# Kernel tuning notes

Hardware: AMD Instinct MI355X
Metric: run time of the kernel (lower is better)

## Reference

```python
import jax, jax.numpy as jnp
import numpy as np
from jax import lax

H = 512   # hidden_size
R = 4     # read heads
W = 32    # memory word size
N = 64    # memory cells
B = 64    # batch
T = 256   # seq len
IFACE = R * W + 3 * W + 5 * R + 3      # 247
HID_C = H + IFACE                       # 759 controller LSTM hidden
IN_C = H + R * W                        # 640 controller LSTM input
EPS = 1e-6


def setup_inputs() -> dict:
    key = jax.random.key(0)
    ks = jax.random.split(key, 7)
    s = 0.05
    return {
        "x": jax.random.normal(ks[0], (B, T, H), jnp.float32),
        "Wih_e": jax.random.normal(ks[1], (4 * H, H), jnp.float32) * s,
        "Whh_e": jax.random.normal(ks[2], (4 * H, H), jnp.float32) * s,
        "b_e": jnp.zeros((4 * H,), jnp.float32),
        "Wih_c": jax.random.normal(ks[3], (4 * HID_C, IN_C), jnp.float32) * s,
        "Whh_c": jax.random.normal(ks[4], (4 * HID_C, HID_C), jnp.float32) * s,
        "b_c": jnp.zeros((4 * HID_C,), jnp.float32),
    }


def lstm_cell(xt, h, c, Wih, Whh, b):
    g = xt @ Wih.T + h @ Whh.T + b
    i, f, gg, o = jnp.split(g, 4, axis=-1)  # PyTorch gate order i,f,g,o
    c = jax.nn.sigmoid(f) * c + jax.nn.sigmoid(i) * jnp.tanh(gg)
    h = jax.nn.sigmoid(o) * jnp.tanh(c)
    return h, c


def content_weights(M, keys, strengths):
    # M: [B,N,W], keys: [B,K,W], strengths: [B,K] -> softmaxed similarity [B,K,N]
    Mn = M * lax.rsqrt(jnp.sum(M * M, -1, keepdims=True) + EPS)
    kn = keys * lax.rsqrt(jnp.sum(keys * keys, -1, keepdims=True) + EPS)
    sim = jnp.einsum('bkw,bnw->bkn', kn, Mn)
    return jax.nn.softmax(sim * strengths[..., None], axis=-1)


def reference(x, Wih_e, Whh_e, b_e, Wih_c, Whh_c, b_c):
    # ---- encoder LSTM over time ----
    def enc_step(carry, xt):
        h, c = carry
        h, c = lstm_cell(xt, h, c, Wih_e, Whh_e, b_e)
        return (h, c), h

    z = jnp.zeros((B, H), x.dtype)
    _, enc = lax.scan(enc_step, (z, z), x.transpose(1, 0, 2))  # [T,B,H]

    # ---- controller LSTM + DNC memory per timestep ----
    eye = jnp.eye(N, dtype=x.dtype)

    def dnc_step(carry, e_t):
        h, c, M, u, p, L, wr, ww, rv = carry
        x_t = jnp.concatenate([e_t, rv], axis=-1)          # [B, H + R*W]
        h, c = lstm_cell(x_t, h, c, Wih_c, Whh_c, b_c)
        out = h[:, :H]
        xi = h[:, H:]                                       # [B, IFACE]
        o = 0
        read_keys = jnp.tanh(xi[:, :R * W].reshape(B, R, W)); o = R * W
        read_str = jax.nn.softplus(xi[:, o:o + R]); o += R
        write_key = jnp.tanh(xi[:, o:o + W]).reshape(B, 1, W); o += W
        write_str = jax.nn.softplus(xi[:, o:o + 1]); o += 1
        erase = jax.nn.sigmoid(xi[:, o:o + W]); o += W
        write_vec = jnp.tanh(xi[:, o:o + W]); o += W
        free_g = jax.nn.sigmoid(xi[:, o:o + R]); o += R
        alloc_g = jax.nn.sigmoid(xi[:, o:o + 1]); o += 1
        write_g = jax.nn.sigmoid(xi[:, o:o + 1]); o += 1
        read_modes = jax.nn.softmax(xi[:, o:o + 3 * R].reshape(B, R, 3), -1)
        # usage + retention
        psi = jnp.prod(1.0 - free_g[..., None] * wr, axis=1)   # [B,N]
        u = (u + ww - u * ww) * psi
        # allocation weighting via sorted usage
        idx = jnp.argsort(u, axis=-1)
        su = jnp.take_along_axis(u, idx, -1)
        cp = jnp.concatenate([jnp.ones((B, 1), u.dtype), jnp.cumprod(su, -1)[:, :-1]], -1)
        a = jnp.take_along_axis((1.0 - su) * cp, jnp.argsort(idx, -1), -1)
        # write weighting
        cw = content_weights(M, write_key, write_str)[:, 0]    # [B,N]
        ww = write_g * (alloc_g * a + (1.0 - alloc_g) * cw)
        # memory write
        M = M * (1.0 - ww[..., None] * erase[:, None, :]) + ww[..., None] * write_vec[:, None, :]
        # temporal link + precedence
        L = (1.0 - ww[:, :, None] - ww[:, None, :]) * L + ww[:, :, None] * p[:, None, :]
        L = L * (1.0 - eye)
        p = (1.0 - jnp.sum(ww, -1, keepdims=True)) * p + ww
        # read weighting: backward, content, forward modes
        cr = content_weights(M, read_keys, read_str)           # [B,R,N]
        fw = jnp.einsum('bnm,brm->brn', L, wr)
        bw = jnp.einsum('bmn,brm->brn', L, wr)
        wr = read_modes[..., 0:1] * bw + read_modes[..., 1:2] * cr + read_modes[..., 2:3] * fw
        rv = jnp.einsum('brn,bnw->brw', wr, M).reshape(B, R * W)
        return (h, c, M, u, p, L, wr, ww, rv), out

    init = (
        jnp.zeros((B, HID_C), x.dtype), jnp.zeros((B, HID_C), x.dtype),
        jnp.zeros((B, N, W), x.dtype), jnp.zeros((B, N), x.dtype),
        jnp.zeros((B, N), x.dtype), jnp.zeros((B, N, N), x.dtype),
        jnp.zeros((B, R, N), x.dtype), jnp.zeros((B, N), x.dtype),
        jnp.zeros((B, R * W), x.dtype),
    )
    _, outs = lax.scan(dnc_step, init, enc)   # [T,B,H]
    return outs.transpose(1, 0, 2)            # dnc_encoded [B,T,H]
```

## Files before the change

kernel.cpp:

```cpp
#include <hip/hip_runtime.h>
#include <math.h>


#define EPSF 1e-6f

__device__ __forceinline__ float sigmoidf_(float x) { return 1.f / (1.f + expf(-x)); }
__device__ __forceinline__ float softplusf_(float x) {
    return (x > 0.f) ? x + log1pf(expf(-x)) : log1pf(expf(x));
}
__device__ __forceinline__ void stg_coh(float* p, float v) {
    __hip_atomic_store(p, v, __ATOMIC_RELAXED, __HIP_MEMORY_SCOPE_AGENT);
}
__device__ __forceinline__ void st_flag(int* p, int v) {
    __hip_atomic_store(p, v, __ATOMIC_RELAXED, __HIP_MEMORY_SCOPE_AGENT);
}
__device__ __forceinline__ int ld_flag(const int* p) {
    return __hip_atomic_load(p, __ATOMIC_RELAXED, __HIP_MEMORY_SCOPE_AGENT);
}
__device__ __forceinline__ void poll256(const int* f, int lane, int tgt) {
    const int* p = f + lane * 32;
    for (;;) {
        int a = ld_flag(p);
        int b = ld_flag(p + 64 * 32);
        int c = ld_flag(p + 128 * 32);
        int d = ld_flag(p + 192 * 32);
        if (__all(min(min(a, b), min(c, d)) >= tgt)) break;
        __builtin_amdgcn_s_sleep(2);
    }
}
__device__ __forceinline__ void pollg(const int* f, int lane, int tgt) {
    const int* p = f + (64 + lane) * 32;
    for (;;) {
        int a = ld_flag(p);
        int b = ld_flag(p + 64 * 32);
        int c = ld_flag(p + 128 * 32);
        if (__all(min(min(a, b), c) >= tgt)) break;
        __builtin_amdgcn_s_sleep(2);
    }
}
__device__ __forceinline__ void pollm(const int* f2, int lane, int tgt) {
    while (!__all(ld_flag(f2 + lane * 32) >= tgt)) __builtin_amdgcn_s_sleep(2);
}

__global__ __launch_bounds__(256) void prep_weights(const float* __restrict__ Whh_c,
                                                    const float* __restrict__ Wih_c,
                                                    float* __restrict__ Wcat) {
    int idx = blockIdx.x * 256 + threadIdx.x;
    if (idx < 3036 * 896) {
        int r = idx / 896, j = idx - r * 896;
        float v;
        if (j < 759) v = Whh_c[r * 759 + j];
        else if (j < 768) v = 0.f;
        else v = Wih_c[r * 640 + 512 + (j - 768)];
        Wcat[idx] = v;
    }
}

__global__ __launch_bounds__(256, 2) void proj_gemm(const float* __restrict__ A,
                                                    const float* __restrict__ W,
                                                    const float* __restrict__ bias,
                                                    float* __restrict__ OUT, int Ncols,
                                                    int wstride, int arow_base, int arow_stride_t,
                                                    int arow_stride_b, int arowlen, int Mrows) {
    __shared__ float As[16 * 68];
    __shared__ float Ws[16 * 68];
    const int tid = threadIdx.x;
    const int ntile = blockIdx.x, mtile = blockIdx.y;
    const int tx = tid & 15, ty = tid >> 4;
    const int lr = tid >> 2;
    const int lk = (tid & 3) * 4;
    const size_t arow =
        (size_t)arow_base + (size_t)mtile * arow_stride_t + (size_t)lr * arow_stride_b;
    const float* aptr = A + arow * arowlen + lk;
    const int wn = ntile * 64 + lr;
    const bool wok = (wn < Ncols);
    const float* wptr = W + (size_t)(wok ? wn : 0) * wstride + lk;
    float acc[4][4] = {};
    for (int kt = 0; kt < 512; kt += 16) {
        float4 av = *(const float4*)(aptr + kt);
        float4 w4l = *(const float4*)(wptr + kt);
        if (!wok) w4l = make_float4(0.f, 0.f, 0.f, 0.f);
        __syncthreads();
        As[(lk + 0) * 68 + lr] = av.x;
        As[(lk + 1) * 68 + lr] = av.y;
        As[(lk + 2) * 68 + lr] = av.z;
        As[(lk + 3) * 68 + lr] = av.w;
        Ws[(lk + 0) * 68 + lr] = w4l.x;
        Ws[(lk + 1) * 68 + lr] = w4l.y;
        Ws[(lk + 2) * 68 + lr] = w4l.z;
        Ws[(lk + 3) * 68 + lr] = w4l.w;
        __syncthreads();
#pragma unroll
        for (int k = 0; k < 16; ++k) {
            float4 a4 = *(const float4*)&As[k * 68 + ty * 4];
            float4 w4 = *(const float4*)&Ws[k * 68 + tx * 4];
            acc[0][0] = fmaf(a4.x, w4.x, acc[0][0]);
            acc[0][1] = fmaf(a4.x, w4.y, acc[0][1]);
            acc[0][2] = fmaf(a4.x, w4.z, acc[0][2]);
            acc[0][3] = fmaf(a4.x, w4.w, acc[0][3]);
            acc[1][0] = fmaf(a4.y, w4.x, acc[1][0]);
            acc[1][1] = fmaf(a4.y, w4.y, acc[1][1]);
            acc[1][2] = fmaf(a4.y, w4.z, acc[1][2]);
            acc[1][3] = fmaf(a4.y, w4.w, acc[1][3]);
            acc[2][0] = fmaf(a4.z, w4.x, acc[2][0]);
            acc[2][1] = fmaf(a4.z, w4.y, acc[2][1]);
            acc[2][2] = fmaf(a4.z, w4.z, acc[2][2]);
            acc[2][3] = fmaf(a4.z, w4.w, acc[2][3]);
            acc[3][0] = fmaf(a4.w, w4.x, acc[3][0]);
            acc[3][1] = fmaf(a4.w, w4.y, acc[3][1]);
            acc[3][2] = fmaf(a4.w, w4.z, acc[3][2]);
            acc[3][3] = fmaf(a4.w, w4.w, acc[3][3]);
        }
    }
    const int col0 = ntile * 64 + tx * 4;
    const int row0 = mtile * 64 + ty * 4;
#pragma unroll
    for (int j = 0; j < 4; ++j) {
        int col = col0 + j;
        if (col < Ncols) {
            float bv = bias[col];
            float4 st = make_float4(acc[0][j] + bv, acc[1][j] + bv, acc[2][j] + bv,
                                    acc[3][j] + bv);
            *(float4*)&OUT[(size_t)col * Mrows + row0] = st;
        }
    }
}

__global__ __launch_bounds__(512, 1) void enc_seq(const float* __restrict__ Whh,
                                                  const float* __restrict__ XPT,
                                                  float* __restrict__ HSE,
                                                  float* __restrict__ CE,
                                                  float* __restrict__ ENC, int M, int t0, int TC,
                                                  int* flags) {
    __shared__ float part[8 * 4 * 64];
    const int tid = threadIdx.x;
    const int bk = blockIdx.x;
    const int lane = tid & 63;
    const int wv = __builtin_amdgcn_readfirstlane(tid >> 6);
    const int q = wv & 3, cidx = wv >> 2;
    const int cell = bk + 256 * cidx;
    const float* __restrict__ w0 = Whh + ((size_t)(0 * 512 + cell)) * 512 + q * 128;
    const float* __restrict__ w1 = Whh + ((size_t)(1 * 512 + cell)) * 512 + q * 128;
    const float* __restrict__ w2 = Whh + ((size_t)(2 * 512 + cell)) * 512 + q * 128;
    const float* __restrict__ w3 = Whh + ((size_t)(3 * 512 + cell)) * 512 + q * 128;
    float c_reg = 0.f;
    if (q == 0) c_reg = CE[cell * 64 + lane];
    for (int tl = 0; tl < TC; ++tl) {
        const int t = t0 + tl;
        const float* rslot = HSE + (size_t)((tl + TC - 1) % TC) * 32768;
        float* wslot = HSE + (size_t)tl * 32768;
        float x0 = 0.f, x1 = 0.f, x2 = 0.f, x3 = 0.f;
        if (q == 0) {
            const int m = tl * 64 + lane;
            x0 = XPT[(size_t)(0 * 512 + cell) * M + m];
            x1 = XPT[(size_t)(1 * 512 + cell) * M + m];
            x2 = XPT[(size_t)(2 * 512 + cell) * M + m];
            x3 = XPT[(size_t)(3 * 512 + cell) * M + m];
        }
        float a0 = 0.f, a1 = 0.f, a2 = 0.f, a3 = 0.f;
        {
            const float4* __restrict__ hx = (const float4*)rslot + q * 32 * 64;
#pragma unroll 8
            for (int i = 0; i < 32; ++i) {
                float4 hv = hx[i * 64 + lane];
                float4 q0 = *(const float4*)&w0[i * 4];
                float4 q1 = *(const float4*)&w1[i * 4];
                float4 q2 = *(const float4*)&w2[i * 4];
                float4 q3 = *(const float4*)&w3[i * 4];
                a0 = fmaf(hv.x, q0.x, a0); a0 = fmaf(hv.y, q0.y, a0);
                a0 = fmaf(hv.z, q0.z, a0); a0 = fmaf(hv.w, q0.w, a0);
                a1 = fmaf(hv.x, q1.x, a1); a1 = fmaf(hv.y, q1.y, a1);
                a1 = fmaf(hv.z, q1.z, a1); a1 = fmaf(hv.w, q1.w, a1);
                a2 = fmaf(hv.x, q2.x, a2); a2 = fmaf(hv.y, q2.y, a2);
                a2 = fmaf(hv.z, q2.z, a2); a2 = fmaf(hv.w, q2.w, a2);
                a3 = fmaf(hv.x, q3.x, a3); a3 = fmaf(hv.y, q3.y, a3);
                a3 = fmaf(hv.z, q3.z, a3); a3 = fmaf(hv.w, q3.w, a3);
            }
        }
        part[(wv * 4 + 0) * 64 + lane] = a0;
        part[(wv * 4 + 1) * 64 + lane] = a1;
        part[(wv * 4 + 2) * 64 + lane] = a2;
        part[(wv * 4 + 3) * 64 + lane] = a3;
        __syncthreads();
        if (q == 0) {
            float g4[4];
#pragma unroll
            for (int g = 0; g < 4; ++g) {
                g4[g] = part[((cidx * 4 + 0) * 4 + g) * 64 + lane] +
                        part[((cidx * 4 + 1) * 4 + g) * 64 + lane] +
                        part[((cidx * 4 + 2) * 4 + g) * 64 + lane] +
                        part[((cidx * 4 + 3) * 4 + g) * 64 + lane];
            }
            float cc = sigmoidf_(g4[1] + x1) * c_reg + sigmoidf_(g4[0] + x0) * tanhf(g4[2] + x2);
            float hh = sigmoidf_(g4[3] + x3) * tanhf(cc);
            c_reg = cc;
            stg_coh(&wslot[(cell >> 2) * 256 + lane * 4 + (cell & 3)], hh);
            ENC[((size_t)t * 64 + lane) * 512 + cell] = hh;
        }
        __syncthreads();
        if (tid == 0) st_flag(flags + bk * 32, tl + 1);
        if (tl + 1 < TC) {
            if (wv == 0) poll256(flags, lane, tl + 1);
            __syncthreads();
        }
    }
    if (q == 0) CE[cell * 64 + lane] = c_reg;
}

__global__ __launch_bounds__(1024, 1) void dnc_seq(
    const float* __restrict__ Wcat, const float* __restrict__ CPT, float* __restrict__ HS,
    float* __restrict__ CC, float* __restrict__ Mg, float* __restrict__ Ug,
    float* __restrict__ Pg, float* __restrict__ WWg, float* __restrict__ Lg,
    float* __restrict__ WRg, float* __restrict__ OUT, int M, int t0, int TC, int* flags) {
    __shared__ float part[16 * 4 * 64];
    __shared__ float M_l[64 * 33];
    __shared__ float L_l[64 * 65];
    __shared__ float act[256];
    __shared__ float wr_l[256];
    __shared__ float u_l[64], p_l[64], ww_l[64], cw_l[64], sM2[64], srt_l[64], asrt_l[64];
    __shared__ int rank_l[64];
    __shared__ float modes_l[12], kss_l[4], scal[4];

    const int tid = threadIdx.x;
    const int bk = blockIdx.x;
    const int lane = tid & 63;
    const int wv = __builtin_amdgcn_readfirstlane(tid >> 6);
    const int q = wv & 3, cidx = wv >> 2;
    const bool machb = (bk < 64);
    const int cell = machb ? 0 : (bk - 64) + 192 * cidx;
    const bool valid = !machb && (cell < 759);
    const int b = bk;
    int* flags2 = flags + 8192;

    const float* __restrict__ wh0 = Wcat + (size_t)(0 * 759 + cell) * 896 + q * 192;
    const float* __restrict__ wh1 = Wcat + (size_t)(1 * 759 + cell) * 896 + q * 192;
    const float* __restrict__ wh2 = Wcat + (size_t)(2 * 759 + cell) * 896 + q * 192;
    const float* __restrict__ wh3 = Wcat + (size_t)(3 * 759 + cell) * 896 + q * 192;
    const float* __restrict__ wr0 = Wcat + (size_t)(0 * 759 + cell) * 896 + 768 + q * 32;
    const float* __restrict__ wr1 = Wcat + (size_t)(1 * 759 + cell) * 896 + 768 + q * 32;
    const float* __restrict__ wr2 = Wcat + (size_t)(2 * 759 + cell) * 896 + 768 + q * 32;
    const float* __restrict__ wr3 = Wcat + (size_t)(3 * 759 + cell) * 896 + 768 + q * 32;

    float c_reg = 0.f;
    if (valid && q == 0) c_reg = CC[cell * 64 + lane];

    if (machb) {
        if (tid < 256) {
#pragma unroll
            for (int i = 0; i < 8; ++i) {
                int e = tid + 256 * i;
                M_l[(e >> 5) * 33 + (e & 31)] = Mg[b * 2048 + e];
            }
#pragma unroll
            for (int i = 0; i < 16; ++i) {
                int e = tid + 256 * i;
                L_l[(e >> 6) * 65 + (e & 63)] = Lg[b * 4096 + e];
            }
            wr_l[tid] = WRg[b * 256 + tid];
        }
        if (tid < 64) {
            u_l[tid] = Ug[b * 64 + tid];
            p_l[tid] = Pg[b * 64 + tid];
            ww_l[tid] = WWg[b * 64 + tid];
        }
        __syncthreads();
    }

    float A0 = 0.f, A1 = 0.f, A2 = 0.f, A3 = 0.f;
    if (valid) {
        const float4* __restrict__ hx = (const float4*)(HS + (size_t)(TC - 1) * 57344) + q * 48 * 64;
#pragma unroll 8
        for (int i = 0; i < 48; ++i) {
            float4 hv = hx[i * 64 + lane];
            float4 u0 = *(const float4*)&wh0[i * 4];
            float4 u1 = *(const float4*)&wh1[i * 4];
            float4 u2 = *(const float4*)&wh2[i * 4];
            float4 u3 = *(const float4*)&wh3[i * 4];
            A0 = fmaf(hv.x, u0.x, A0); A0 = fmaf(hv.y, u0.y, A0);
            A0 = fmaf(hv.z, u0.z, A0); A0 = fmaf(hv.w, u0.w, A0);
            A1 = fmaf(hv.x, u1.x, A1); A1 = fmaf(hv.y, u1.y, A1);
            A1 = fmaf(hv.z, u1.z, A1); A1 = fmaf(hv.w, u1.w, A1);
            A2 = fmaf(hv.x, u2.x, A2); A2 = fmaf(hv.y, u2.y, A2);
            A2 = fmaf(hv.z, u2.z, A2); A2 = fmaf(hv.w, u2.w, A2);
            A3 = fmaf(hv.x, u3.x, A3); A3 = fmaf(hv.y, u3.y, A3);
            A3 = fmaf(hv.z, u3.z, A3); A3 = fmaf(hv.w, u3.w, A3);
        }
    }

    for (int tl = 0; tl < TC; ++tl) {
        const int t = t0 + tl;
        const bool last = (tl + 1 == TC);
        const float* rslot = HS + (size_t)((tl + TC - 1) % TC) * 57344;
        float* wslot = HS + (size_t)tl * 57344;
        if (!machb) {
            float b0 = 0.f, b1 = 0.f, b2 = 0.f, b3 = 0.f;
            float p0 = 0.f, p1 = 0.f, p2 = 0.f, p3 = 0.f;
            if (valid && q == 0) {
                const int m = tl * 64 + lane;
                p0 = CPT[(size_t)(0 * 759 + cell) * M + m];
                p1 = CPT[(size_t)(1 * 759 + cell) * M + m];
                p2 = CPT[(size_t)(2 * 759 + cell) * M + m];
                p3 = CPT[(size_t)(3 * 759 + cell) * M + m];
            }
            if (valid) {
                const float4* __restrict__ hx = (const float4*)rslot + (192 + q * 8) * 64;
#pragma unroll
                for (int i = 0; i < 8; ++i) {
                    float4 hv = hx[i * 64 + lane];
                    float4 u0 = *(const float4*)&wr0[i * 4];
                    float4 u1 = *(const float4*)&wr1[i * 4];
                    float4 u2 = *(const float4*)&wr2[i * 4];
                    float4 u3 = *(const float4*)&wr3[i * 4];
                    b0 = fmaf(hv.x, u0.x, b0); b0 = fmaf(hv.y, u0.y, b0);
                    b0 = fmaf(hv.z, u0.z, b0); b0 = fmaf(hv.w, u0.w, b0);
                    b1 = fmaf(hv.x, u1.x, b1); b1 = fmaf(hv.y, u1.y, b1);
                    b1 = fmaf(hv.z, u1.z, b1); b1 = fmaf(hv.w, u1.w, b1);
                    b2 = fmaf(hv.x, u2.x, b2); b2 = fmaf(hv.y, u2.y, b2);
                    b2 = fmaf(hv.z, u2.z, b2); b2 = fmaf(hv.w, u2.w, b2);
                    b3 = fmaf(hv.x, u3.x, b3); b3 = fmaf(hv.y, u3.y, b3);
                    b3 = fmaf(hv.z, u3.z, b3); b3 = fmaf(hv.w, u3.w, b3);
                }
            }
            part[(wv * 4 + 0) * 64 + lane] = A0 + b0;
            part[(wv * 4 + 1) * 64 + lane] = A1 + b1;
            part[(wv * 4 + 2) * 64 + lane] = A2 + b2;
            part[(wv * 4 + 3) * 64 + lane] = A3 + b3;
            __syncthreads();
            if (valid && q == 0) {
                float g4[4];
#pragma unroll
                for (int g = 0; g < 4; ++g) {
                    g4[g] = part[((cidx * 4 + 0) * 4 + g) * 64 + lane] +
                            part[((cidx * 4 + 1) * 4 + g) * 64 + lane] +
                            part[((cidx * 4 + 2) * 4 + g) * 64 + lane] +
                            part[((cidx * 4 + 3) * 4 + g) * 64 + lane];
                }
                float cc =
                    sigmoidf_(g4[1] + p1) * c_reg + sigmoidf_(g4[0] + p0) * tanhf(g4[2] + p2);
                float hh = sigmoidf_(g4[3] + p3) * tanhf(cc);
                c_reg = cc;
                stg_coh(&wslot[(cell >> 2) * 256 + lane * 4 + (cell & 3)], hh);
                if (cell < 512) OUT[(size_t)lane * 131072 + (size_t)t * 512 + cell] = hh;
            }
            __syncthreads();
            if (tid == 0) st_flag(flags + bk * 32, tl + 1);
            if (!last) {
                if (wv == 0) pollg(flags, lane, tl + 1);
                __syncthreads();
                A0 = A1 = A2 = A3 = 0.f;
                if (valid) {
                    const float4* __restrict__ hx = (const float4*)wslot + q * 48 * 64;
#pragma unroll 8
                    for (int i = 0; i < 48; ++i) {
                        float4 hv = hx[i * 64 + lane];
                        float4 u0 = *(const float4*)&wh0[i * 4];
                        float4 u1 = *(const float4*)&wh1[i * 4];
                        float4 u2 = *(const float4*)&wh2[i * 4];
                        float4 u3 = *(const float4*)&wh3[i * 4];
                        A0 = fmaf(hv.x, u0.x, A0); A0 = fmaf(hv.y, u0.y, A0);
                        A0 = fmaf(hv.z, u0.z, A0); A0 = fmaf(hv.w, u0.w, A0);
                        A1 = fmaf(hv.x, u1.x, A1); A1 = fmaf(hv.y, u1.y, A1);
                        A1 = fmaf(hv.z, u1.z, A1); A1 = fmaf(hv.w, u1.w, A1);
                        A2 = fmaf(hv.x, u2.x, A2); A2 = fmaf(hv.y, u2.y, A2);
                        A2 = fmaf(hv.z, u2.z, A2); A2 = fmaf(hv.w, u2.w, A2);
                        A3 = fmaf(hv.x, u3.x, A3); A3 = fmaf(hv.y, u3.y, A3);
                        A3 = fmaf(hv.z, u3.z, A3); A3 = fmaf(hv.w, u3.w, A3);
                    }
                }
                if (wv == 0) pollm(flags2, lane, tl + 1);
                __syncthreads();
            }
        } else {
            if (wv == 0) pollg(flags, lane, tl + 1);
            __syncthreads();
            if (tid < 247) {
                float v = wslot[(128 + (tid >> 2)) * 256 + b * 4 + (tid & 3)];
                float a;
                if (tid < 128) a = tanhf(v);
                else if (tid < 132) a = softplusf_(v);
                else if (tid < 164) a = tanhf(v);
                else if (tid == 164) a = softplusf_(v);
                else if (tid < 197) a = sigmoidf_(v);
                else if (tid < 229) a = tanhf(v);
                else if (tid < 235) a = sigmoidf_(v);
                else a = v;
                act[tid] = a;
            }
            __syncthreads();
            if (tid < 4) {
                float m0 = act[235 + 3 * tid], m1 = act[236 + 3 * tid], m2 = act[237 + 3 * tid];
                float mx = fmaxf(m0, fmaxf(m1, m2));
                float e0 = expf(m0 - mx), e1 = expf(m1 - mx), e2 = expf(m2 - mx);
                float s = e0 + e1 + e2;
                modes_l[3 * tid] = e0 / s;
                modes_l[3 * tid + 1] = e1 / s;
                modes_l[3 * tid + 2] = e2 / s;
                float ks = 0.f;
                for (int w = 0; w < 32; ++w) {
                    float kk = act[tid * 32 + w];
                    ks = fmaf(kk, kk, ks);
                }
                kss_l[tid] = ks;
            }
            if (tid == 64) {
                float s = 0.f;
                for (int w = 0; w < 32; ++w) {
                    float kk = act[132 + w];
                    s = fmaf(kk, kk, s);
                }
                scal[0] = s;
            }
            if (tid < 64) {
                float psi = 1.f;
#pragma unroll
                for (int r = 0; r < 4; ++r) psi *= 1.f - act[229 + r] * wr_l[r * 64 + tid];
                float un = u_l[tid], wwn = ww_l[tid];
                u_l[tid] = (un + wwn - un * wwn) * psi;
                float s2 = 0.f;
                for (int w = 0; w < 32; ++w) {
                    float mm = M_l[tid * 33 + w];
                    s2 = fmaf(mm, mm, s2);
                }
                sM2[tid] = s2;
            }
            __syncthreads();
            if (tid < 64) {
                float un = u_l[tid];
                int rk = 0;
                for (int m = 0; m < 64; ++m) {
                    float um = u_l[m];
                    rk += (um < un) || (um == un && m < tid);
                }
                srt_l[rk] = un;
                rank_l[tid] = rk;
            }
            __syncthreads();
            if (tid < 64) {
                float v = srt_l[tid];
                float incl = v;
#pragma unroll
                for (int off = 1; off < 64; off <<= 1) {
                    float o = __shfl_up(incl, off);
                    if (tid >= off) incl *= o;
                }
                float excl = __shfl_up(incl, 1);
                if (tid == 0) excl = 1.f;
                asrt_l[tid] = (1.f - v) * excl;
                float dot = 0.f;
                for (int w = 0; w < 32; ++w) dot = fmaf(act[132 + w], M_l[tid * 33 + w], dot);
                float logit = dot * rsqrtf(sM2[tid] + EPSF) * rsqrtf(scal[0] + EPSF) * act[164];
                float mx = logit;
#pragma unroll
                for (int off = 32; off; off >>= 1) mx = fmaxf(mx, __shfl_xor(mx, off));
                float e = expf(logit - mx);
                float s = e;
#pragma unroll
                for (int off = 32; off; off >>= 1) s += __shfl_xor(s, off);
                cw_l[tid] = e / s;
            }
            __syncthreads();
            if (tid < 64) {
                float a = asrt_l[rank_l[tid]];
                float agv = act[233], wgv = act[234];
                float wn = wgv * (agv * a + (1.f - agv) * cw_l[tid]);
                ww_l[tid] = wn;
                float s = wn;
#pragma unroll
                for (int off = 32; off; off >>= 1) s += __shfl_xor(s, off);
                if (tid == 0) scal[1] = s;
            }
            __syncthreads();
            if (tid < 256) {
#pragma unroll
                for (int i = 0; i < 8; ++i) {
                    int e = tid + 256 * i;
                    int n = e >> 5, w = e & 31;
                    float wwn = ww_l[n];
                    M_l[n * 33 + w] =
                        M_l[n * 33 + w] * (1.f - wwn * act[165 + w]) + wwn * act[197 + w];
                }
#pragma unroll
                for (int i = 0; i < 16; ++i) {
                    int e = tid + 256 * i;
                    int n = e >> 6, m = e & 63;
                    float Lv = L_l[n * 65 + m];
                    Lv = (1.f - ww_l[n] - ww_l[m]) * Lv + ww_l[n] * p_l[m];
                    L_l[n * 65 + m] = (n == m) ? 0.f : Lv;
                }
            }
            __syncthreads();
            if (tid < 64) {
                p_l[tid] = (1.f - scal[1]) * p_l[tid] + ww_l[tid];
                float s2 = 0.f;
                for (int w = 0; w < 32; ++w) {
                    float mm = M_l[tid * 33 + w];
                    s2 = fmaf(mm, mm, s2);
                }
                sM2[tid] = s2;
            }
            __syncthreads();
            float wrn = 0.f;
            if (tid < 256) {
                const int r = wv;
                const int n = lane;
                float dot = 0.f;
                for (int w = 0; w < 32; ++w) dot = fmaf(act[r * 32 + w], M_l[n * 33 + w], dot);
                float logit = dot * rsqrtf(sM2[n] + EPSF) * rsqrtf(kss_l[r] + EPSF) * act[128 + r];
                float mx = logit;
#pragma unroll
                for (int off = 32; off; off >>= 1) mx = fmaxf(mx, __shfl_xor(mx, off));
                float e = expf(logit - mx);
                float s = e;
#pragma unroll
                for (int off = 32; off; off >>= 1) s += __shfl_xor(s, off);
                float cr = e / s;
                float fw = 0.f, bw = 0.f;
                for (int m = 0; m < 64; ++m) {
                    float wrm = wr_l[r * 64 + m];
                    fw = fmaf(L_l[n * 65 + m], wrm, fw);
                    bw = fmaf(L_l[m * 65 + n], wrm, bw);
                }
                wrn = modes_l[r * 3] * bw + modes_l[r * 3 + 1] * cr + modes_l[r * 3 + 2] * fw;
            }
            __syncthreads();
            if (tid < 256) wr_l[tid] = wrn;
            __syncthreads();
            if (tid < 128) {
                const int r = tid >> 5, w = tid & 31;
                float rv = 0.f;
                for (int n = 0; n < 64; ++n) rv = fmaf(wr_l[r * 64 + n], M_l[n * 33 + w], rv);
                stg_coh(&wslot[(192 + (tid >> 2)) * 256 + b * 4 + (tid & 3)], rv);
            }
            __syncthreads();
            if (tid == 0) st_flag(flags2 + bk * 32, tl + 1);
        }
    }
    if (valid && q == 0) CC[cell * 64 + lane] = c_reg;
    if (machb) {
        if (tid < 256) {
#pragma unroll
            for (int i = 0; i < 8; ++i) {
                int e = tid + 256 * i;
                Mg[b * 2048 + e] = M_l[(e >> 5) * 33 + (e & 31)];
            }
#pragma unroll
            for (int i = 0; i < 16; ++i) {
                int e = tid + 256 * i;
                Lg[b * 4096 + e] = L_l[(e >> 6) * 65 + (e & 63)];
            }
            WRg[b * 256 + tid] = wr_l[tid];
        }
        if (tid < 64) {
            Ug[b * 64 + tid] = u_l[tid];
            Pg[b * 64 + tid] = p_l[tid];
            WWg[b * 64 + tid] = ww_l[tid];
        }
    }
}

extern "C" void kernel_launch(void* const* d_in, const int* in_sizes, int n_in, void* d_out,
                              int out_size, void* d_ws, size_t ws_size, hipStream_t stream) {
    const float* x = (const float*)d_in[0];
    const float* Wih_e = (const float*)d_in[1];
    const float* Whh_e = (const float*)d_in[2];
    const float* b_e = (const float*)d_in[3];
    const float* Wih_c = (const float*)d_in[4];
    const float* Whh_c = (const float*)d_in[5];
    const float* b_c = (const float*)d_in[6];
    float* out = (float*)d_out;
    float* ws = (float*)d_ws;

    int TC = 32;
    while (TC > 2) {
        size_t need =
            ((size_t)11612096 + (size_t)TC * 415488 + (size_t)(512 / TC) * 16384) * 4;
        if (need <= ws_size) break;
        TC >>= 1;
    }
    const int nch = 256 / TC;
    const int M = TC * 64;

    size_t off = 0;
    float* XPT = ws + off; off += (size_t)2048 * M;
    float* CPT = ws + off; off += (size_t)3036 * M;
    float* Wcat = ws + off; off += (size_t)3036 * 896;
    float* ENC = ws + off; off += (size_t)256 * 64 * 512;
    size_t zoff = off;
    float* HSE = ws + off; off += (size_t)TC * 32768;
    float* CE = ws + off; off += 512 * 64;
    float* HS = ws + off; off += (size_t)TC * 57344;
    float* CC = ws + off; off += 759 * 64;
    float* Mg = ws + off; off += 64 * 2048;
    float* Ug = ws + off; off += 64 * 64;
    float* Pg = ws + off; off += 64 * 64;
    float* WWg = ws + off; off += 64 * 64;
    float* Lg = ws + off; off += 64 * 4096;
    float* WRg = ws + off; off += 64 * 256;
    int* BAR = (int*)(ws + off); off += (size_t)2 * nch * 16384;
    size_t zbytes = (off - zoff) * 4;

    hipMemsetAsync(ws + zoff, 0, zbytes, stream);
    prep_weights<<<dim3((3036 * 896 + 255) / 256), dim3(256), 0, stream>>>(Whh_c, Wih_c, Wcat);
    for (int c = 0; c < nch; ++c) {
        proj_gemm<<<dim3(32, TC), dim3(256), 0, stream>>>(x, Wih_e, b_e, XPT, 2048, 512, c * TC,
                                                          1, 256, 512, M);
        enc_seq<<<dim3(256), dim3(512), 0, stream>>>(Whh_e, XPT, HSE, CE, ENC, M, c * TC, TC,
                                                     BAR + (size_t)c * 16384);
    }
    for (int c = 0; c < nch; ++c) {
        proj_gemm<<<dim3(48, TC), dim3(256), 0, stream>>>(ENC, Wih_c, b_c, CPT, 3036, 640,
                                                          c * TC * 64, 64, 1, 512, M);
        dnc_seq<<<dim3(256), dim3(1024), 0, stream>>>(Wcat, CPT, HS, CC, Mg, Ug, Pg, WWg, Lg,
                                                      WRg, out, M, c * TC, TC,
                                                      BAR + (size_t)(nch + c) * 16384);
    }
}
```

Baseline: 8.430 ms.

## Move sequence output writes to separate kernels and trim DNC step barriers

Scattered per-step global writes of encoder and controller hidden states (ENC, OUT) are removed from the recurrent kernels and done afterwards by coalesced copy kernels that read the chunk's hidden-state ring buffer. In dnc_seq the cell mapping is changed so the interface rows land contiguously, which lets memory blocks poll only the flags of the producing blocks. Next-step projection loads are prefetched before the wait. Several __syncthreads phases in the memory update are merged by computing usage, rank, allocation and norms in fewer passes. The sequential critical path gets shorter, at the cost of extra kernel launches and a dependence on the ring buffer holding every step of the chunk.

```diff
diff --git a/kernel.cpp b/kernel.cpp
--- a/kernel.cpp
+++ b/kernel.cpp
@@ -37,6 +37,10 @@
         if (__all(min(min(a, b), c) >= tgt)) break;
         __builtin_amdgcn_s_sleep(2);
     }
+}
+__device__ __forceinline__ void pollx(const int* f, int lane, int tgt) {
+    const int* p = f + (192 + (lane < 62 ? lane : 61)) * 32;
+    while (!__all(ld_flag(p) >= tgt)) __builtin_amdgcn_s_sleep(2);
 }
 __device__ __forceinline__ void pollm(const int* f2, int lane, int tgt) {
     while (!__all(ld_flag(f2 + lane * 32) >= tgt)) __builtin_amdgcn_s_sleep(2);
@@ -126,11 +130,25 @@
     }
 }
 
+__global__ __launch_bounds__(256) void enc_emit(const float* __restrict__ HSE,
+                                                float* __restrict__ ENC, int t0) {
+    const int tl = blockIdx.x, bgrp = blockIdx.y;
+    const int c4 = threadIdx.x & 127, b = bgrp * 2 + (threadIdx.x >> 7);
+    float4 v = *(const float4*)&HSE[(size_t)tl * 32768 + c4 * 256 + b * 4];
+    *(float4*)&ENC[((size_t)(t0 + tl) * 64 + b) * 512 + c4 * 4] = v;
+}
+__global__ __launch_bounds__(256) void out_emit(const float* __restrict__ HS,
+                                                float* __restrict__ OUT, int t0) {
+    const int tl = blockIdx.x, bgrp = blockIdx.y;
+    const int c4 = threadIdx.x & 127, b = bgrp * 2 + (threadIdx.x >> 7);
+    float4 v = *(const float4*)&HS[(size_t)tl * 57344 + c4 * 256 + b * 4];
+    *(float4*)&OUT[(size_t)b * 131072 + (size_t)(t0 + tl) * 512 + c4 * 4] = v;
+}
+
 __global__ __launch_bounds__(512, 1) void enc_seq(const float* __restrict__ Whh,
                                                   const float* __restrict__ XPT,
                                                   float* __restrict__ HSE,
-                                                  float* __restrict__ CE,
-                                                  float* __restrict__ ENC, int M, int t0, int TC,
+                                                  float* __restrict__ CE, int M, int TC,
                                                   int* flags) {
     __shared__ float part[8 * 4 * 64];
     const int tid = threadIdx.x;
@@ -146,7 +164,6 @@
     float c_reg = 0.f;
     if (q == 0) c_reg = CE[cell * 64 + lane];
     for (int tl = 0; tl < TC; ++tl) {
-        const int t = t0 + tl;
         const float* rslot = HSE + (size_t)((tl + TC - 1) % TC) * 32768;
         float* wslot = HSE + (size_t)tl * 32768;
         float x0 = 0.f, x1 = 0.f, x2 = 0.f, x3 = 0.f;
@@ -195,7 +212,6 @@
             float hh = sigmoidf_(g4[3] + x3) * tanhf(cc);
             c_reg = cc;
             stg_coh(&wslot[(cell >> 2) * 256 + lane * 4 + (cell & 3)], hh);
-            ENC[((size_t)t * 64 + lane) * 512 + cell] = hh;
         }
         __syncthreads();
         if (tid == 0) st_flag(flags + bk * 32, tl + 1);
@@ -211,14 +227,13 @@
     const float* __restrict__ Wcat, const float* __restrict__ CPT, float* __restrict__ HS,
     float* __restrict__ CC, float* __restrict__ Mg, float* __restrict__ Ug,
     float* __restrict__ Pg, float* __restrict__ WWg, float* __restrict__ Lg,
-    float* __restrict__ WRg, float* __restrict__ OUT, int M, int t0, int TC, int* flags) {
+    float* __restrict__ WRg, int M, int TC, int* flags) {
     __shared__ float part[16 * 4 * 64];
     __shared__ float M_l[64 * 33];
     __shared__ float L_l[64 * 65];
     __shared__ float act[256];
     __shared__ float wr_l[256];
-    __shared__ float u_l[64], p_l[64], ww_l[64], cw_l[64], sM2[64], srt_l[64], asrt_l[64];
-    __shared__ int rank_l[64];
+    __shared__ float u_l[64], p_l[64], ww_l[64], sM2[64], srt_l[64], asrt_l[64];
     __shared__ float modes_l[12], kss_l[4], scal[4];
 
     const int tid = threadIdx.x;
@@ -227,8 +242,9 @@
     const int wv = __builtin_amdgcn_readfirstlane(tid >> 6);
     const int q = wv & 3, cidx = wv >> 2;
     const bool machb = (bk < 64);
-    const int cell = machb ? 0 : (bk - 64) + 192 * cidx;
-    const bool valid = !machb && (cell < 759);
+    const int cell_raw = machb ? 0 : (bk - 64) * 4 + cidx;
+    const bool valid = !machb && (cell_raw < 759);
+    const int cell = valid ? cell_raw : 0;
     const int b = bk;
     int* flags2 = flags + 8192;
 
@@ -266,6 +282,13 @@
         __syncthreads();
     }
 
+    float cp0 = 0.f, cp1 = 0.f, cp2 = 0.f, cp3 = 0.f;
+    if (valid && q == 0) {
+        cp0 = CPT[(size_t)(0 * 759 + cell) * M + lane];
+        cp1 = CPT[(size_t)(1 * 759 + cell) * M + lane];
+        cp2 = CPT[(size_t)(2 * 759 + cell) * M + lane];
+        cp3 = CPT[(size_t)(3 * 759 + cell) * M + lane];
+    }
     float A0 = 0.f, A1 = 0.f, A2 = 0.f, A3 = 0.f;
     if (valid) {
         const float4* __restrict__ hx = (const float4*)(HS + (size_t)(TC - 1) * 57344) + q * 48 * 64;
@@ -288,20 +311,11 @@
     }
 
     for (int tl = 0; tl < TC; ++tl) {
-        const int t = t0 + tl;
         const bool last = (tl + 1 == TC);
         const float* rslot = HS + (size_t)((tl + TC - 1) % TC) * 57344;
         float* wslot = HS + (size_t)tl * 57344;
         if (!machb) {
             float b0 = 0.f, b1 = 0.f, b2 = 0.f, b3 = 0.f;
-            float p0 = 0.f, p1 = 0.f, p2 = 0.f, p3 = 0.f;
-            if (valid && q == 0) {
-                const int m = tl * 64 + lane;
-                p0 = CPT[(size_t)(0 * 759 + cell) * M + m];
-                p1 = CPT[(size_t)(1 * 759 + cell) * M + m];
-                p2 = CPT[(size_t)(2 * 759 + cell) * M + m];
-                p3 = CPT[(size_t)(3 * 759 + cell) * M + m];
-            }
             if (valid) {
                 const float4* __restrict__ hx = (const float4*)rslot + (192 + q * 8) * 64;
 #pragma unroll
@@ -336,17 +350,24 @@
                             part[((cidx * 4 + 3) * 4 + g) * 64 + lane];
                 }
                 float cc =
-                    sigmoidf_(g4[1] + p1) * c_reg + sigmoidf_(g4[0] + p0) * tanhf(g4[2] + p2);
-                float hh = sigmoidf_(g4[3] + p3) * tanhf(cc);
+                    sigmoidf_(g4[1] + cp1) * c_reg + sigmoidf_(g4[0] + cp0) * tanhf(g4[2] + cp2);
+                float hh = sigmoidf_(g4[3] + cp3) * tanhf(cc);
                 c_reg = cc;
-                stg_coh(&wslot[(cell >> 2) * 256 + lane * 4 + (cell & 3)], hh);
-                if (cell < 512) OUT[(size_t)lane * 131072 + (size_t)t * 512 + cell] = hh;
+                stg_coh(&wslot[(bk - 64) * 256 + lane * 4 + cidx], hh);
             }
             __syncthreads();
             if (tid == 0) st_flag(flags + bk * 32, tl + 1);
             if (!last) {
                 if (wv == 0) pollg(flags, lane, tl + 1);
                 __syncthreads();
+                float np0 = 0.f, np1 = 0.f, np2 = 0.f, np3 = 0.f;
+                if (valid && q == 0) {
+                    const int m = (tl + 1) * 64 + lane;
+                    np0 = CPT[(size_t)(0 * 759 + cell) * M + m];
+                    np1 = CPT[(size_t)(1 * 759 + cell) * M + m];
+                    np2 = CPT[(size_t)(2 * 759 + cell) * M + m];
+                    np3 = CPT[(size_t)(3 * 759 + cell) * M + m];
+                }
                 A0 = A1 = A2 = A3 = 0.f;
                 if (valid) {
                     const float4* __restrict__ hx = (const float4*)wslot + q * 48 * 64;
@@ -367,11 +388,12 @@
                         A3 = fmaf(hv.z, u3.z, A3); A3 = fmaf(hv.w, u3.w, A3);
                     }
                 }
+                cp0 = np0; cp1 = np1; cp2 = np2; cp3 = np3;
                 if (wv == 0) pollm(flags2, lane, tl + 1);
                 __syncthreads();
             }
         } else {
-            if (wv == 0) pollg(flags, lane, tl + 1);
+            if (wv == 0) pollx(flags, lane, tl + 1);
             __syncthreads();
             if (tid < 247) {
                 float v = wslot[(128 + (tid >> 2)) * 256 + b * 4 + (tid & 3)];
@@ -386,36 +408,7 @@
                 else a = v;
                 act[tid] = a;
             }
-            __syncthreads();
-            if (tid < 4) {
-                float m0 = act[235 + 3 * tid], m1 = act[236 + 3 * tid], m2 = act[237 + 3 * tid];
-                float mx = fmaxf(m0, fmaxf(m1, m2));
-                float e0 = expf(m0 - mx), e1 = expf(m1 - mx), e2 = expf(m2 - mx);
-                float s = e0 + e1 + e2;
-                modes_l[3 * tid] = e0 / s;
-                modes_l[3 * tid + 1] = e1 / s;
-                modes_l[3 * tid + 2] = e2 / s;
-                float ks = 0.f;
-                for (int w = 0; w < 32; ++w) {
-                    float kk = act[tid * 32 + w];
-                    ks = fmaf(kk, kk, ks);
-                }
-                kss_l[tid] = ks;
-            }
-            if (tid == 64) {
-                float s = 0.f;
-                for (int w = 0; w < 32; ++w) {
-                    float kk = act[132 + w];
-                    s = fmaf(kk, kk, s);
-                }
-                scal[0] = s;
-            }
             if (tid < 64) {
-                float psi = 1.f;
-#pragma unroll
-                for (int r = 0; r < 4; ++r) psi *= 1.f - act[229 + r] * wr_l[r * 64 + tid];
-                float un = u_l[tid], wwn = ww_l[tid];
-                u_l[tid] = (un + wwn - un * wwn) * psi;
                 float s2 = 0.f;
                 for (int w = 0; w < 32; ++w) {
                     float mm = M_l[tid * 33 + w];
@@ -425,17 +418,42 @@
             }
             __syncthreads();
             if (tid < 64) {
-                float un = u_l[tid];
+                if (tid < 4) {
+                    float m0 = act[235 + 3 * tid], m1 = act[236 + 3 * tid],
+                          m2 = act[237 + 3 * tid];
+                    float mx = fmaxf(m0, fmaxf(m1, m2));
+                    float e0 = expf(m0 - mx), e1 = expf(m1 - mx), e2 = expf(m2 - mx);
+                    float s = e0 + e1 + e2;
+                    modes_l[3 * tid] = e0 / s;
+                    modes_l[3 * tid + 1] = e1 / s;
+                    modes_l[3 * tid + 2] = e2 / s;
+                    float ks = 0.f;
+                    for (int w = 0; w < 32; ++w) {
+                        float kk = act[tid * 32 + w];
+                        ks = fmaf(kk, kk, ks);
+                    }
+                    kss_l[tid] = ks;
+                }
+                if (tid == 4) {
+                    float s = 0.f;
+                    for (int w = 0; w < 32; ++w) {
+                        float kk = act[132 + w];
+                        s = fmaf(kk, kk, s);
+                    }
+                    scal[0] = s;
+                }
+                float psi = 1.f;
+#pragma unroll
+                for (int r = 0; r < 4; ++r) psi *= 1.f - act[229 + r] * wr_l[r * 64 + tid];
+                float un = u_l[tid], wwo = ww_l[tid];
+                float unew = (un + wwo - un * wwo) * psi;
+                u_l[tid] = unew;
                 int rk = 0;
                 for (int m = 0; m < 64; ++m) {
                     float um = u_l[m];
-                    rk += (um < un) || (um == un && m < tid);
-                }
-                srt_l[rk] = un;
-                rank_l[tid] = rk;
-            }
-            __syncthreads();
-            if (tid < 64) {
+                    rk += (um < unew) || (um == unew && m < tid);
+                }
+                srt_l[rk] = unew;
                 float v = srt_l[tid];
                 float incl = v;
 #pragma unroll
@@ -456,18 +474,15 @@
                 float s = e;
 #pragma unroll
                 for (int off = 32; off; off >>= 1) s += __shfl_xor(s, off);
-                cw_l[tid] = e / s;
-            }
-            __syncthreads();
-            if (tid < 64) {
-                float a = asrt_l[rank_l[tid]];
+                float cw = e / s;
+                float a = asrt_l[rk];
                 float agv = act[233], wgv = act[234];
-                float wn = wgv * (agv * a + (1.f - agv) * cw_l[tid]);
+                float wn = wgv * (agv * a + (1.f - agv) * cw);
                 ww_l[tid] = wn;
-                float s = wn;
-#pragma unroll
-                for (int off = 32; off; off >>= 1) s += __shfl_xor(s, off);
-                if (tid == 0) scal[1] = s;
+                float sw = wn;
+#pragma unroll
+                for (int off = 32; off; off >>= 1) sw += __shfl_xor(sw, off);
+                if (tid == 0) scal[1] = sw;
             }
             __syncthreads();
             if (tid < 256) {
@@ -489,23 +504,19 @@
                 }
             }
             __syncthreads();
-            if (tid < 64) {
-                p_l[tid] = (1.f - scal[1]) * p_l[tid] + ww_l[tid];
-                float s2 = 0.f;
-                for (int w = 0; w < 32; ++w) {
-                    float mm = M_l[tid * 33 + w];
-                    s2 = fmaf(mm, mm, s2);
-                }
-                sM2[tid] = s2;
-            }
-            __syncthreads();
             float wrn = 0.f;
             if (tid < 256) {
                 const int r = wv;
                 const int n = lane;
+                if (r == 0) p_l[n] = (1.f - scal[1]) * p_l[n] + ww_l[n];
+                float s2 = 0.f;
+                for (int w = 0; w < 32; ++w) {
+                    float mm = M_l[n * 33 + w];
+                    s2 = fmaf(mm, mm, s2);
+                }
                 float dot = 0.f;
                 for (int w = 0; w < 32; ++w) dot = fmaf(act[r * 32 + w], M_l[n * 33 + w], dot);
-                float logit = dot * rsqrtf(sM2[n] + EPSF) * rsqrtf(kss_l[r] + EPSF) * act[128 + r];
+                float logit = dot * rsqrtf(s2 + EPSF) * rsqrtf(kss_l[r] + EPSF) * act[128 + r];
                 float mx = logit;
 #pragma unroll
                 for (int off = 32; off; off >>= 1) mx = fmaxf(mx, __shfl_xor(mx, off));
@@ -604,14 +615,15 @@
     for (int c = 0; c < nch; ++c) {
         proj_gemm<<<dim3(32, TC), dim3(256), 0, stream>>>(x, Wih_e, b_e, XPT, 2048, 512, c * TC,
                                                           1, 256, 512, M);
-        enc_seq<<<dim3(256), dim3(512), 0, stream>>>(Whh_e, XPT, HSE, CE, ENC, M, c * TC, TC,
+        enc_seq<<<dim3(256), dim3(512), 0, stream>>>(Whh_e, XPT, HSE, CE, M, TC,
                                                      BAR + (size_t)c * 16384);
+        enc_emit<<<dim3(TC, 32), dim3(256), 0, stream>>>(HSE, ENC, c * TC);
     }
     for (int c = 0; c < nch; ++c) {
         proj_gemm<<<dim3(48, TC), dim3(256), 0, stream>>>(ENC, Wih_c, b_c, CPT, 3036, 640,
                                                           c * TC * 64, 64, 1, 512, M);
         dnc_seq<<<dim3(256), dim3(1024), 0, stream>>>(Wcat, CPT, HS, CC, Mg, Ug, Pg, WWg, Lg,
-                                                      WRg, out, M, c * TC, TC,
-                                                      BAR + (size_t)(nch + c) * 16384);
-    }
-}
+                                                      WRg, M, TC, BAR + (size_t)(nch + c) * 16384);
+        out_emit<<<dim3(TC, 32), dim3(256), 0, stream>>>(HS, out, c * TC);
+    }
+}
```

Result: faster. 8.099 ms (-3.9%).
